# Performance work log

Measured on AMD Instinct MI355X. Metric: run time of the kernel, lower is better.

The kernel has to match this reference:

```python
import jax, jax.numpy as jnp
import numpy as np

B, S, E, H = 1, 8192, 1024, 16
D = E // H
SEG_LENS = [2048, 4096, 8192]
DILATIONS = [1, 2, 4]


def setup_inputs() -> dict:
    key = jax.random.key(0)
    k0, k1, k2 = jax.random.split(key, 3)
    sc_in = 1.0 / np.sqrt(E)
    return {
        "x": jax.random.normal(k0, (B, S, E), jnp.float32),
        "w_qkv": jax.random.normal(k1, (3 * E, E), jnp.float32) * sc_in,
        "b_qkv": jnp.zeros((3 * E,), jnp.float32),
        "w_out": jax.random.normal(k2, (E, E), jnp.float32) * sc_in,
        "b_out": jnp.zeros((E,), jnp.float32),
    }


def _sdpa(q, k, v):
    # q,k,v: [B,H,N,D]; standard scaled dot-product attention (non-causal)
    scale = 1.0 / np.sqrt(q.shape[-1])
    scores = jnp.einsum('bhqd,bhkd->bhqk', q, k) * scale
    probs = jax.nn.softmax(scores, axis=-1)
    return jnp.einsum('bhqk,bhkd->bhqd', probs, v)


def reference(x, w_qkv, b_qkv, w_out, b_out):
    # QKV projection: torch Linear is x @ W^T + b
    qkv = x @ w_qkv.T + b_qkv                       # [B,S,3E]
    qkv = qkv.reshape(B, S, 3, H, D).transpose(2, 0, 3, 1, 4)  # [3,B,H,S,D]
    q, k, v = qkv[0], qkv[1], qkv[2]

    seg_outputs = []
    for seg_len, dil in zip(SEG_LENS, DILATIONS):
        if seg_len > S:
            continue
        if dil > 1:
            n = min(seg_len, S // dil)
            pos = np.arange(0, n * dil, dil)        # strided dilated gather
        else:
            pos = np.arange(seg_len)                # leading segment
        o = _sdpa(q[:, :, pos], k[:, :, pos], v[:, :, pos])
        # scatter back to full length (zero elsewhere); also handles zero-padding
        full = jnp.zeros((B, H, S, D), x.dtype).at[:, :, pos, :].set(o)
        seg_outputs.append(full)

    if len(seg_outputs) == 0:
        out = jnp.zeros((B, H, S, D), x.dtype)
    else:
        out = seg_outputs[0]
        for so in seg_outputs[1:]:
            out = out + so
        out = out / len(seg_outputs)                # stack(...).mean(0)

    out = out.transpose(0, 2, 1, 3).reshape(B, S, E)
    return out @ w_out.T + b_out
```

## Files before the change

### kernel.cpp

```cpp
#include <hip/hip_runtime.h>


typedef __attribute__((ext_vector_type(8))) short bf16x8;
typedef __attribute__((ext_vector_type(4))) float f32x4;

#define MFMA(a, b, c) __builtin_amdgcn_mfma_f32_16x16x32_bf16((a), (b), (c), 0, 0, 0)

#if __has_builtin(__builtin_amdgcn_exp2f)
#define EXP2(x) __builtin_amdgcn_exp2f(x)
#else
#define EXP2(x) exp2f(x)
#endif

static __device__ __forceinline__ unsigned short f2bf(float f) {
  unsigned int u = __float_as_uint(f);
  unsigned int r = (u + 0x7FFFu + ((u >> 16) & 1u)) >> 16;
  return (unsigned short)r;
}

__global__ void cvt_f32_bf16(const float* __restrict__ in,
                             unsigned short* __restrict__ out, int n8) {
  int i = blockIdx.x * blockDim.x + threadIdx.x;
  if (i >= n8) return;
  const float4* p = (const float4*)in + (size_t)i * 2;
  float4 a = p[0];
  float4 b = p[1];
  union { bf16x8 v; unsigned short u[8]; } o;
  o.u[0] = f2bf(a.x); o.u[1] = f2bf(a.y); o.u[2] = f2bf(a.z); o.u[3] = f2bf(a.w);
  o.u[4] = f2bf(b.x); o.u[5] = f2bf(b.y); o.u[6] = f2bf(b.z); o.u[7] = f2bf(b.w);
  *((bf16x8*)out + i) = o.v;
}

template <int EPILOGUE>
__global__ __launch_bounds__(256, 2) void gemm_bt(
    const unsigned short* __restrict__ A, const unsigned short* __restrict__ B,
    const float* __restrict__ bias, void* __restrict__ Cout, int N, int K) {
  __shared__ unsigned short At[128 * 32];
  __shared__ unsigned short Bt[128 * 32];
  const int tid = threadIdx.x;
  const int wave = tid >> 6, lane = tid & 63;
  const int quad = lane >> 4, lc = lane & 15;
  const int wm = (wave >> 1) * 64, wn = (wave & 1) * 64;
  const int m0 = blockIdx.x * 128, n0 = blockIdx.y * 128;

  f32x4 acc[4][4] = {};

  for (int k0 = 0; k0 < K; k0 += 32) {
    __syncthreads();
#pragma unroll
    for (int issue = 0; issue < 2; ++issue) {
      const int cbase = issue * 256 + wave * 64;
      const int c = cbase + lane;
      const int row = c >> 2, col8 = (c & 3) * 8;
      __builtin_amdgcn_global_load_lds(
          (const __attribute__((address_space(1))) void*)&A[(size_t)(m0 + row) * K + k0 + col8],
          (__attribute__((address_space(3))) void*)&At[cbase * 8], 16, 0, 0);
      __builtin_amdgcn_global_load_lds(
          (const __attribute__((address_space(1))) void*)&B[(size_t)(n0 + row) * K + k0 + col8],
          (__attribute__((address_space(3))) void*)&Bt[cbase * 8], 16, 0, 0);
    }
    __syncthreads();
    bf16x8 af[4], bfr[4];
#pragma unroll
    for (int t = 0; t < 4; ++t)
      af[t] = *(const bf16x8*)&At[(wm + t * 16 + lc) * 32 + quad * 8];
#pragma unroll
    for (int t = 0; t < 4; ++t)
      bfr[t] = *(const bf16x8*)&Bt[(wn + t * 16 + lc) * 32 + quad * 8];
#pragma unroll
    for (int i = 0; i < 4; ++i)
#pragma unroll
      for (int j = 0; j < 4; ++j)
        acc[i][j] = MFMA(af[i], bfr[j], acc[i][j]);
  }

#pragma unroll
  for (int i = 0; i < 4; ++i) {
#pragma unroll
    for (int j = 0; j < 4; ++j) {
      const int gcol = n0 + wn + j * 16 + lc;
      const float bs = bias[gcol];
#pragma unroll
      for (int r = 0; r < 4; ++r) {
        const int grow = m0 + wm + i * 16 + quad * 4 + r;
        const float v = acc[i][j][r] + bs;
        if (EPILOGUE == 0) {
          const int which = gcol >> 10, rem = gcol & 1023;
          const int hh = rem >> 6, d = rem & 63;
          const float vs = (which == 0) ? v * 0.18033688f : v;
          ((unsigned short*)Cout)[(((size_t)(which * 16 + hh)) * 8192 + grow) * 64 + d] = f2bf(vs);
        } else {
          ((float*)Cout)[(size_t)grow * N + gcol] = v;
        }
      }
    }
  }
}

__global__ void transpose_v(const unsigned short* __restrict__ v,
                            unsigned short* __restrict__ vt1,
                            unsigned short* __restrict__ vt2,
                            unsigned short* __restrict__ vt3) {
  __shared__ unsigned short Tt[64 * 72];
  const int tid = threadIdx.x;
  const int h = blockIdx.y;
  const int bx = blockIdx.x;
  const unsigned short* src = v + (size_t)h * 8192 * 64;
  unsigned short* dst;
  int dil, Nk, t0;
  if (bx < 32)      { dst = vt1; dil = 1; Nk = 2048; t0 = bx; }
  else if (bx < 96) { dst = vt2; dil = 2; Nk = 4096; t0 = bx - 32; }
  else              { dst = vt3; dil = 4; Nk = 2048; t0 = bx - 96; }
  dst += (size_t)h * 64 * Nk;
  const int j0 = t0 * 64;
#pragma unroll
  for (int it = 0; it < 2; ++it) {
    const int slot = tid + it * 256;
    const int jj = slot >> 3, c8 = (slot & 7) * 8;
    *(bf16x8*)&Tt[jj * 72 + c8] =
        *(const bf16x8*)&src[(size_t)(j0 + jj) * dil * 64 + c8];
  }
  __syncthreads();
  const int d = tid >> 2, pg = (tid & 3) * 16;
  union { bf16x8 v2[2]; unsigned short u[16]; } ob;
#pragma unroll
  for (int t = 0; t < 16; ++t) {
    const int pos = pg + t;
    const int w = pos & 31;
    const int jj = (pos & 32) | (((w >> 2) & 1) * 16 + (w >> 3) * 4 + (w & 3));
    ob.u[t] = Tt[jj * 72 + d];
  }
  *(bf16x8*)&dst[(size_t)d * Nk + j0 + pg] = ob.v2[0];
  *(bf16x8*)&dst[(size_t)d * Nk + j0 + pg + 8] = ob.v2[1];
}

__global__ __launch_bounds__(256, 2) void flash_all(
    const unsigned short* __restrict__ qkvb,
    const unsigned short* __restrict__ vt1, float* __restrict__ o1,
    const unsigned short* __restrict__ vt2, float* __restrict__ o2,
    const unsigned short* __restrict__ vt3, float* __restrict__ o3) {
  __shared__ unsigned short Smem[2 * 64 * 64];
  unsigned short* Kt = Smem;
  unsigned short* Vt = Smem + 64 * 64;

  const int bx = blockIdx.x;
  int z, h, qt;
  if ((bx & 1) == 0) { const int i = bx >> 1; z = 1; h = i >> 4; qt = i & 15; }
  else { const int j = bx >> 1; z = (j & 1) ? 2 : 0; const int i = j >> 1; h = i >> 3; qt = i & 7; }
  const int Nk = (z == 1) ? 4096 : 2048;
  const int dil = 1 << z;
  const unsigned short* vt = (z == 0) ? vt1 : (z == 1) ? vt2 : vt3;
  float* o = (z == 0) ? o1 : (z == 1) ? o2 : o3;

  const int tid = threadIdx.x;
  const int wave = tid >> 6, lane = tid & 63;
  const int quad = lane >> 4, lc = lane & 15;

  const unsigned short* qh = qkvb + (size_t)h * 8192 * 64;
  const unsigned short* kh = qkvb + (size_t)(16 + h) * 8192 * 64;
  const unsigned short* vh = vt + (size_t)h * 64 * Nk;

  bf16x8 qf[4][2];
#pragma unroll
  for (int mb = 0; mb < 4; ++mb) {
    const size_t qrow = (size_t)(qt * 256 + wave * 64 + mb * 16 + lc) * dil;
    qf[mb][0] = *(const bf16x8*)&qh[qrow * 64 + quad * 8];
    qf[mb][1] = *(const bf16x8*)&qh[qrow * 64 + quad * 8 + 32];
  }

  union { bf16x8 v; unsigned short u[8]; } one_u;
#pragma unroll
  for (int t = 0; t < 8; ++t) one_u.u[t] = 0x3F80;
  const bf16x8 vone = one_u.v;

  f32x4 oacc[4][4] = {};
  f32x4 lacc[4] = {};

  const int srow = tid >> 3, scol = tid & 7;
  const int swz = (scol ^ (srow & 7)) * 8;

  bf16x8 kg0 = *(const bf16x8*)&kh[(size_t)(srow * dil) * 64 + scol * 8];
  bf16x8 kg1 = *(const bf16x8*)&kh[(size_t)((srow + 32) * dil) * 64 + scol * 8];
  bf16x8 vg0 = *(const bf16x8*)&vh[(size_t)srow * Nk + scol * 8];
  bf16x8 vg1 = *(const bf16x8*)&vh[(size_t)(srow + 32) * Nk + scol * 8];

  for (int kb = 0; kb < Nk; kb += 64) {
    __syncthreads();
    *(bf16x8*)&Kt[srow * 64 + swz] = kg0;
    *(bf16x8*)&Kt[(srow + 32) * 64 + swz] = kg1;
    *(bf16x8*)&Vt[srow * 64 + swz] = vg0;
    *(bf16x8*)&Vt[(srow + 32) * 64 + swz] = vg1;
    __syncthreads();

    if (kb + 64 < Nk) {
      const int nk = kb + 64;
      kg0 = *(const bf16x8*)&kh[(size_t)((nk + srow) * dil) * 64 + scol * 8];
      kg1 = *(const bf16x8*)&kh[(size_t)((nk + srow + 32) * dil) * 64 + scol * 8];
      vg0 = *(const bf16x8*)&vh[(size_t)srow * Nk + nk + scol * 8];
      vg1 = *(const bf16x8*)&vh[(size_t)(srow + 32) * Nk + nk + scol * 8];
    }

#pragma unroll
    for (int ks = 0; ks < 2; ++ks) {
      f32x4 st[2][4];
#pragma unroll
      for (int t = 0; t < 2; ++t) {
        const int row = (ks * 2 + t) * 16 + lc;
        const bf16x8 ka0 = *(const bf16x8*)&Kt[row * 64 + ((quad ^ (lc & 7)) * 8)];
        const bf16x8 ka1 = *(const bf16x8*)&Kt[row * 64 + (((4 + quad) ^ (lc & 7)) * 8)];
#pragma unroll
        for (int mb = 0; mb < 4; ++mb) {
          f32x4 zz = {};
          zz = MFMA(ka0, qf[mb][0], zz);
          st[t][mb] = MFMA(ka1, qf[mb][1], zz);
        }
      }

      bf16x8 pb[4];
#pragma unroll
      for (int mb = 0; mb < 4; ++mb) {
        union { bf16x8 v; unsigned int u[4]; } pu;
#pragma unroll
        for (int t = 0; t < 2; ++t) {
          const unsigned int a0 = __float_as_uint(EXP2(st[t][mb][0])) + 0x8000u;
          const unsigned int a1 = __float_as_uint(EXP2(st[t][mb][1])) + 0x8000u;
          const unsigned int a2 = __float_as_uint(EXP2(st[t][mb][2])) + 0x8000u;
          const unsigned int a3 = __float_as_uint(EXP2(st[t][mb][3])) + 0x8000u;
          pu.u[t * 2 + 0] = __builtin_amdgcn_perm(a1, a0, 0x07060302u);
          pu.u[t * 2 + 1] = __builtin_amdgcn_perm(a3, a2, 0x07060302u);
        }
        pb[mb] = pu.v;
      }

#pragma unroll
      for (int nb = 0; nb < 4; ++nb) {
        const int vrow = nb * 16 + lc;
        const bf16x8 va = *(const bf16x8*)&Vt[vrow * 64 + (((ks * 4 + quad) ^ (lc & 7)) * 8)];
#pragma unroll
        for (int mb = 0; mb < 4; ++mb)
          oacc[mb][nb] = MFMA(va, pb[mb], oacc[mb][nb]);
      }
#pragma unroll
      for (int mb = 0; mb < 4; ++mb) lacc[mb] = MFMA(vone, pb[mb], lacc[mb]);
    }
  }

  __syncthreads();
  float* W = (float*)Smem + wave * 16 * 64;
  const int g = lane >> 2, s4 = lane & 3;
#pragma unroll
  for (int mb = 0; mb < 4; ++mb) {
    const float inv = 1.0f / (3.0f * lacc[mb][0]);
#pragma unroll
    for (int nb = 0; nb < 4; ++nb) {
      const int c = nb * 4 + quad;
      const int cs = (c & 8) | ((c & 7) ^ (lc & 7));
      f32x4 val = oacc[mb][nb];
      val *= inv;
      *(f32x4*)&W[lc * 64 + cs * 4] = val;
    }
    const size_t base = (size_t)(qt * 256 + wave * 64 + mb * 16 + g) * 1024 +
                        (size_t)((bx & 1) ? ((bx >> 1) >> 1) >> 3 : (bx >> 1) >> 4) * 64 + s4 * 16;
#pragma unroll
    for (int c2 = 0; c2 < 4; ++c2) {
      const int c = s4 * 4 + c2;
      const int cs = (c & 8) | ((c & 7) ^ (g & 7));
      *(float4*)&o[base + c2 * 4] = *(const float4*)&W[g * 64 + cs * 4];
    }
  }
}

__global__ void combine(const float* __restrict__ o1, const float* __restrict__ o2,
                        const float* __restrict__ o3,
                        unsigned short* __restrict__ a3b) {
  const int idx = blockIdx.x * 256 + threadIdx.x;
  const int s = idx >> 7, e = (idx & 127) * 8;
  float acc[8] = {};
  if (s < 2048) {
    const float* p = &o1[(size_t)s * 1024 + e];
#pragma unroll
    for (int t = 0; t < 8; ++t) acc[t] += p[t];
  }
  if (!(s & 1)) {
    const float* p = &o2[(size_t)(s >> 1) * 1024 + e];
#pragma unroll
    for (int t = 0; t < 8; ++t) acc[t] += p[t];
  }
  if (!(s & 3)) {
    const float* p = &o3[(size_t)(s >> 2) * 1024 + e];
#pragma unroll
    for (int t = 0; t < 8; ++t) acc[t] += p[t];
  }
  union { bf16x8 v; unsigned short u[8]; } ob;
#pragma unroll
  for (int t = 0; t < 8; ++t) ob.u[t] = f2bf(acc[t]);
  *(bf16x8*)&a3b[(size_t)s * 1024 + e] = ob.v;
}

extern "C" void kernel_launch(void* const* d_in, const int* in_sizes, int n_in,
                              void* d_out, int out_size, void* d_ws, size_t ws_size,
                              hipStream_t stream) {
  const float* x     = (const float*)d_in[0];
  const float* w_qkv = (const float*)d_in[1];
  const float* b_qkv = (const float*)d_in[2];
  const float* w_out = (const float*)d_in[3];
  const float* b_out = (const float*)d_in[4];
  float* out = (float*)d_out;

  char* ws = (char*)d_ws;
  unsigned short* qkvb  = (unsigned short*)(ws);
  float*          o1    = (float*)(ws + 33554432);
  float*          o3    = (float*)(ws + 41943040);
  unsigned short* vt1   = (unsigned short*)(ws + 50331648);
  unsigned short* vt2   = (unsigned short*)(ws + 54525952);
  unsigned short* vt3   = (unsigned short*)(ws + 62914560);
  float*          o2    = (float*)(ws + 67108864);
  unsigned short* wqkvb = (unsigned short*)(ws + 83886080);
  unsigned short* woutb = (unsigned short*)(ws + 90177536);
  unsigned short* xb    = (unsigned short*)(ws + 92274688);
  unsigned short* a3b   = xb;

  cvt_f32_bf16<<<dim3(8388608 / 8 / 256), dim3(256), 0, stream>>>(x, xb, 8388608 / 8);
  cvt_f32_bf16<<<dim3(3145728 / 8 / 256), dim3(256), 0, stream>>>(w_qkv, wqkvb, 3145728 / 8);
  cvt_f32_bf16<<<dim3(1048576 / 8 / 256), dim3(256), 0, stream>>>(w_out, woutb, 1048576 / 8);

  gemm_bt<0><<<dim3(64, 24), dim3(256), 0, stream>>>(xb, wqkvb, b_qkv, qkvb, 3072, 1024);

  transpose_v<<<dim3(128, 16), dim3(256), 0, stream>>>(qkvb + (size_t)32 * 8192 * 64,
                                                       vt1, vt2, vt3);

  flash_all<<<dim3(512), dim3(256), 0, stream>>>(qkvb, vt1, o1, vt2, o2, vt3, o3);

  combine<<<dim3(4096), dim3(256), 0, stream>>>(o1, o2, o3, a3b);

  gemm_bt<1><<<dim3(64, 8), dim3(256), 0, stream>>>(a3b, woutb, b_out, out, 1024, 1024);
}
```

Before: 341.0 us.

## Split the 4096-key segment attention into two KV halves for load balance

The dilation-2 segment's query tiles, which previously scanned 4096 keys, are now each split into two blocks of 2048 keys. Every one of the 768 flash blocks now does equal work, and the per-half unnormalized outputs and row sums go to separate buffers. The combine kernel merges the two halves by normalizing with the summed row sums. Launch bounds are raised to 3 blocks per CU so all blocks can be resident at once. This adds extra fp32 partial-output traffic and workspace aliasing, and raises register pressure that could cause spills.

```diff
diff --git a/kernel.cpp b/kernel.cpp
--- a/kernel.cpp
+++ b/kernel.cpp
@@ -134,23 +134,36 @@
   *(bf16x8*)&dst[(size_t)d * Nk + j0 + pg + 8] = ob.v2[1];
 }
 
-__global__ __launch_bounds__(256, 2) void flash_all(
+__global__ __launch_bounds__(256, 3) void flash_all(
     const unsigned short* __restrict__ qkvb,
     const unsigned short* __restrict__ vt1, float* __restrict__ o1,
-    const unsigned short* __restrict__ vt2, float* __restrict__ o2,
+    const unsigned short* __restrict__ vt2, float* __restrict__ o2a,
+    float* __restrict__ o2b, float* __restrict__ l2a, float* __restrict__ l2b,
     const unsigned short* __restrict__ vt3, float* __restrict__ o3) {
   __shared__ unsigned short Smem[2 * 64 * 64];
   unsigned short* Kt = Smem;
   unsigned short* Vt = Smem + 64 * 64;
 
   const int bx = blockIdx.x;
-  int z, h, qt;
-  if ((bx & 1) == 0) { const int i = bx >> 1; z = 1; h = i >> 4; qt = i & 15; }
-  else { const int j = bx >> 1; z = (j & 1) ? 2 : 0; const int i = j >> 1; h = i >> 3; qt = i & 7; }
+  const int i = bx / 3;
+  const int r = bx - 3 * i;
+  int z, h, qt, kb0;
+  const unsigned short* vt;
+  float* o;
+  float* lout = nullptr;
+  if (r < 2) {
+    z = 1; h = i >> 4; qt = i & 15; kb0 = r * 2048;
+    vt = vt2; o = (r == 0) ? o2a : o2b; lout = (r == 0) ? l2a : l2b;
+  } else if (i < 128) {
+    z = 0; h = i >> 3; qt = i & 7; kb0 = 0; vt = vt1; o = o1;
+  } else {
+    const int j = i - 128;
+    z = 2; h = j >> 3; qt = j & 7; kb0 = 0; vt = vt3; o = o3;
+  }
   const int Nk = (z == 1) ? 4096 : 2048;
+  const int kbEnd = kb0 + 2048;
   const int dil = 1 << z;
-  const unsigned short* vt = (z == 0) ? vt1 : (z == 1) ? vt2 : vt3;
-  float* o = (z == 0) ? o1 : (z == 1) ? o2 : o3;
+  const bool split = (r < 2);
 
   const int tid = threadIdx.x;
   const int wave = tid >> 6, lane = tid & 63;
@@ -179,12 +192,12 @@
   const int srow = tid >> 3, scol = tid & 7;
   const int swz = (scol ^ (srow & 7)) * 8;
 
-  bf16x8 kg0 = *(const bf16x8*)&kh[(size_t)(srow * dil) * 64 + scol * 8];
-  bf16x8 kg1 = *(const bf16x8*)&kh[(size_t)((srow + 32) * dil) * 64 + scol * 8];
-  bf16x8 vg0 = *(const bf16x8*)&vh[(size_t)srow * Nk + scol * 8];
-  bf16x8 vg1 = *(const bf16x8*)&vh[(size_t)(srow + 32) * Nk + scol * 8];
-
-  for (int kb = 0; kb < Nk; kb += 64) {
+  bf16x8 kg0 = *(const bf16x8*)&kh[(size_t)((kb0 + srow) * dil) * 64 + scol * 8];
+  bf16x8 kg1 = *(const bf16x8*)&kh[(size_t)((kb0 + srow + 32) * dil) * 64 + scol * 8];
+  bf16x8 vg0 = *(const bf16x8*)&vh[(size_t)srow * Nk + kb0 + scol * 8];
+  bf16x8 vg1 = *(const bf16x8*)&vh[(size_t)(srow + 32) * Nk + kb0 + scol * 8];
+
+  for (int kb = kb0; kb < kbEnd; kb += 64) {
     __syncthreads();
     *(bf16x8*)&Kt[srow * 64 + swz] = kg0;
     *(bf16x8*)&Kt[(srow + 32) * 64 + swz] = kg1;
@@ -192,7 +205,7 @@
     *(bf16x8*)&Vt[(srow + 32) * 64 + swz] = vg1;
     __syncthreads();
 
-    if (kb + 64 < Nk) {
+    if (kb + 64 < kbEnd) {
       const int nk = kb + 64;
       kg0 = *(const bf16x8*)&kh[(size_t)((nk + srow) * dil) * 64 + scol * 8];
       kg1 = *(const bf16x8*)&kh[(size_t)((nk + srow + 32) * dil) * 64 + scol * 8];
@@ -250,7 +263,9 @@
   const int g = lane >> 2, s4 = lane & 3;
 #pragma unroll
   for (int mb = 0; mb < 4; ++mb) {
-    const float inv = 1.0f / (3.0f * lacc[mb][0]);
+    const float inv = split ? 1.0f : 1.0f / (3.0f * lacc[mb][0]);
+    if (split && quad == 0)
+      lout[(size_t)h * 4096 + qt * 256 + wave * 64 + mb * 16 + lc] = lacc[mb][0];
 #pragma unroll
     for (int nb = 0; nb < 4; ++nb) {
       const int c = nb * 4 + quad;
@@ -260,7 +275,7 @@
       *(f32x4*)&W[lc * 64 + cs * 4] = val;
     }
     const size_t base = (size_t)(qt * 256 + wave * 64 + mb * 16 + g) * 1024 +
-                        (size_t)((bx & 1) ? ((bx >> 1) >> 1) >> 3 : (bx >> 1) >> 4) * 64 + s4 * 16;
+                        (size_t)h * 64 + s4 * 16;
 #pragma unroll
     for (int c2 = 0; c2 < 4; ++c2) {
       const int c = s4 * 4 + c2;
@@ -270,7 +285,9 @@
   }
 }
 
-__global__ void combine(const float* __restrict__ o1, const float* __restrict__ o2,
+__global__ void combine(const float* __restrict__ o1,
+                        const float* __restrict__ o2a, const float* __restrict__ o2b,
+                        const float* __restrict__ l2a, const float* __restrict__ l2b,
                         const float* __restrict__ o3,
                         unsigned short* __restrict__ a3b) {
   const int idx = blockIdx.x * 256 + threadIdx.x;
@@ -282,9 +299,14 @@
     for (int t = 0; t < 8; ++t) acc[t] += p[t];
   }
   if (!(s & 1)) {
-    const float* p = &o2[(size_t)(s >> 1) * 1024 + e];
-#pragma unroll
-    for (int t = 0; t < 8; ++t) acc[t] += p[t];
+    const int j = s >> 1, hh = e >> 6;
+    const float la = l2a[(size_t)hh * 4096 + j];
+    const float lb = l2b[(size_t)hh * 4096 + j];
+    const float w = 1.0f / (3.0f * (la + lb));
+    const float* pa = &o2a[(size_t)j * 1024 + e];
+    const float* pb = &o2b[(size_t)j * 1024 + e];
+#pragma unroll
+    for (int t = 0; t < 8; ++t) acc[t] += (pa[t] + pb[t]) * w;
   }
   if (!(s & 3)) {
     const float* p = &o3[(size_t)(s >> 2) * 1024 + e];
@@ -314,11 +336,14 @@
   unsigned short* vt1   = (unsigned short*)(ws + 50331648);
   unsigned short* vt2   = (unsigned short*)(ws + 54525952);
   unsigned short* vt3   = (unsigned short*)(ws + 62914560);
-  float*          o2    = (float*)(ws + 67108864);
+  float*          o2a   = (float*)(ws + 67108864);
   unsigned short* wqkvb = (unsigned short*)(ws + 83886080);
+  float*          l2a   = (float*)(ws + 83886080);
+  float*          l2b   = (float*)(ws + 84148224);
   unsigned short* woutb = (unsigned short*)(ws + 90177536);
   unsigned short* xb    = (unsigned short*)(ws + 92274688);
-  unsigned short* a3b   = xb;
+  float*          o2b   = (float*)(ws + 92274688);
+  unsigned short* a3b   = (unsigned short*)(ws + 50331648);
 
   cvt_f32_bf16<<<dim3(8388608 / 8 / 256), dim3(256), 0, stream>>>(x, xb, 8388608 / 8);
   cvt_f32_bf16<<<dim3(3145728 / 8 / 256), dim3(256), 0, stream>>>(w_qkv, wqkvb, 3145728 / 8);
@@ -329,9 +354,10 @@
   transpose_v<<<dim3(128, 16), dim3(256), 0, stream>>>(qkvb + (size_t)32 * 8192 * 64,
                                                        vt1, vt2, vt3);
 
-  flash_all<<<dim3(512), dim3(256), 0, stream>>>(qkvb, vt1, o1, vt2, o2, vt3, o3);
-
-  combine<<<dim3(4096), dim3(256), 0, stream>>>(o1, o2, o3, a3b);
+  flash_all<<<dim3(768), dim3(256), 0, stream>>>(qkvb, vt1, o1, vt2, o2a, o2b,
+                                                 l2a, l2b, vt3, o3);
+
+  combine<<<dim3(4096), dim3(256), 0, stream>>>(o1, o2a, o2b, l2a, l2b, o3, a3b);
 
   gemm_bt<1><<<dim3(64, 8), dim3(256), 0, stream>>>(a3b, woutb, b_out, out, 1024, 1024);
 }
```

Result: slower. 349.4 us (+2.5%).
